# Kernel optimization log

Measured on AMD Instinct MI355X. Metric: run time of the kernel, lower is better.

## Reference

```python
import jax, jax.numpy as jnp
import numpy as np

EPS = 1e-6  # flax nn.LayerNorm default epsilon


def excl_cumsum(a, axis):
    c = jnp.roll(jnp.cumsum(a, axis=axis), 1, axis=axis)
    idx = [slice(None)] * a.ndim
    idx[axis] = slice(0, 1)
    return c.at[tuple(idx)].set(0.0)


def mixed_chunk_attn(q, k, v, n_chunks):
    # Mixed chunk linear attention (https://arxiv.org/pdf/2202.10447.pdf)
    if n_chunks == 1:
        mask = jnp.tri(q.shape[1], q.shape[1], -1, dtype=q.dtype)
        qk = jnp.einsum('bls,bms->blm', q, k) * mask
        return jnp.einsum('blm,bme->ble', qk, v)
    B, L = q.shape[:2]
    C = L // n_chunks
    qc = q.reshape(B, n_chunks, C, -1)
    kc = k.reshape(B, n_chunks, C, -1)
    vc = v.reshape(B, n_chunks, C, -1)
    # global linear attention across chunks (exclusive prefix of kv states)
    kv = excl_cumsum(jnp.einsum('bgcs,bgce->bgse', kc, vc), axis=1)
    glob = jnp.einsum('bgcs,bgse->bgce', qc, kv)
    # local strictly-causal quadratic attention within each chunk
    mask = jnp.tri(C, C, -1, dtype=q.dtype)
    qk = jnp.einsum('bgns,bgms->bgnm', qc, kc) * mask
    loc = jnp.einsum('bgnm,bgme->bgne', qk, vc)
    return (glob + loc).reshape(B, L, -1)


def ln_normalize(x):
    mu = jnp.mean(x, axis=-1, keepdims=True)
    var = jnp.mean(jnp.square(x - mu), axis=-1, keepdims=True)
    return (x - mu) * jax.lax.rsqrt(var + EPS)


def fwblock(x, labels, weights, W1, b1, W2, b2, ln_scale, ln_bias, Wu, bu, step_sizes, n_chunks):
    B, L, D = x.shape
    F = W1.shape[1]

    # slow-weight forward with zero perturbations; grad wrt perturbations gives
    # per-token gradients at each layer's output (rank-one fast-weight updates).
    def slow_loss(p1, p3, p_scale, p_bias):
        h1 = x @ W1 + b1 + p1                    # FWDense(4D) + output perturbation
        h2 = jnp.square(jax.nn.relu(h1))         # FWSquaredRelu (paramless)
        h3 = h2 @ W2 + b2 + p3                   # FWDense(D) + output perturbation
        h4 = ln_normalize(h3) * (ln_scale + p_scale) + (ln_bias + p_bias)
        logits = h4 @ Wu + bu
        ll = -jnp.sum(jax.nn.log_softmax(logits) * labels, axis=-1)
        loss = jnp.sum(weights * ll) / jnp.maximum(jnp.sum(weights), 1e-8)
        return loss, h2

    zeros = (jnp.zeros((B, L, F), x.dtype), jnp.zeros((B, L, D), x.dtype),
             jnp.zeros((B, L, D), x.dtype), jnp.zeros((B, L, D), x.dtype))
    (g1, g3, g_scale, g_bias), h2_slow = jax.grad(
        slow_loss, argnums=(0, 1, 2, 3), has_aux=True)(*zeros)

    # fast-weight forward: rank-one weight updates expressed as causal linear attn
    x1 = x @ W1 + b1 - step_sizes[0] * mixed_chunk_attn(x, x, g1, n_chunks)
    x2 = jnp.square(jax.nn.relu(x1))             # step_sizes[1] unused (no params)
    x3 = x2 @ W2 + b2 - step_sizes[2] * mixed_chunk_attn(x2, h2_slow, g3, n_chunks)
    fast_scale = ln_scale - step_sizes[3] * excl_cumsum(g_scale, axis=1)
    fast_bias = ln_bias - step_sizes[3] * excl_cumsum(g_bias, axis=1)
    x4 = ln_normalize(x3) * fast_scale + fast_bias
    return x4 @ Wu + bu


def setup_inputs():
    key = jax.random.key(0)
    ks = jax.random.split(key, 6)
    B, L, D, V = 2, 2048, 1024, 8192
    F = 4 * D
    x = jax.random.normal(ks[0], (B, L, D), jnp.float32)
    labels = jax.random.uniform(ks[1], (B, L, V), jnp.float32)
    weights = jnp.ones((B, L), jnp.float32)
    W1 = jax.random.normal(ks[2], (D, F), jnp.float32) / np.sqrt(D).astype(np.float32)
    b1 = jnp.zeros((F,), jnp.float32)
    W2 = jax.random.normal(ks[3], (F, D), jnp.float32) / np.sqrt(F).astype(np.float32)
    b2 = jnp.zeros((D,), jnp.float32)
    ln_scale = jnp.ones((D,), jnp.float32)
    ln_bias = jnp.zeros((D,), jnp.float32)
    Wu = jax.random.normal(ks[4], (D, V), jnp.float32) / np.sqrt(D).astype(np.float32)
    bu = jnp.zeros((V,), jnp.float32)
    step_sizes = jnp.full((4,), 0.01, jnp.float32)
    return dict(x=x, labels=labels, weights=weights, W1=W1, b1=b1, W2=W2, b2=b2,
                ln_scale=ln_scale, ln_bias=ln_bias, Wu=Wu, bu=bu,
                step_sizes=step_sizes, n_chunks=16)


def reference(x, labels, weights, W1, b1, W2, b2, ln_scale, ln_bias, Wu, bu, step_sizes, n_chunks):
    return fwblock(x, labels, weights, W1, b1, W2, b2, ln_scale, ln_bias, Wu, bu, step_sizes, n_chunks)
```

## Files before the change

### kernel.cpp

```cpp
#include <hip/hip_runtime.h>
#include <cstdint>

typedef unsigned short ushort_t;
typedef __bf16 bf16x8 __attribute__((ext_vector_type(8)));
typedef float f32x4 __attribute__((ext_vector_type(4)));
typedef ushort_t us8 __attribute__((ext_vector_type(8)));

__device__ __forceinline__ ushort_t f2bf(float f) {
  union { float f; unsigned int u; } v; v.f = f;
  unsigned int u = v.u;
  unsigned int r = (u + 0x7fffu + ((u >> 16) & 1u)) >> 16;
  return (ushort_t)r;
}
__device__ __forceinline__ float bf2f(ushort_t u) {
  union { unsigned int u; float f; } v; v.u = ((unsigned int)u) << 16; return v.f;
}

#define GLOAD16(gp, lp)                                                              \
  __builtin_amdgcn_global_load_lds(                                                  \
      reinterpret_cast<const __attribute__((address_space(1))) unsigned int*>(       \
          reinterpret_cast<uintptr_t>(gp)),                                          \
      reinterpret_cast<__attribute__((address_space(3))) unsigned int*>(             \
          reinterpret_cast<uintptr_t>(lp)),                                          \
      16, 0, 0)

struct GemmP {
  const ushort_t* A; const ushort_t* B;
  int M, N, K;
  long long sA, sB;
  float* outf;   long long sOutF;
  ushort_t* outb; long long sOutB;
  ushort_t* outb2;
  const float* bias;
  const float* auxf; long long sAuxF;
  const ushort_t* auxb;
  const float* steps;
  float* part; int ksplit, Kc, Tt;
};

template <int EPI>
__global__ __launch_bounds__(512, 2) void gemm256(GemmP p) {
  const int nwg = gridDim.x * gridDim.y;
  const int orig = blockIdx.y * gridDim.x + blockIdx.x;
  const int xcd = orig & 7, loc = orig >> 3;
  const int q8 = nwg >> 3, r8 = nwg & 7;
  const int wg = (xcd < r8) ? (xcd * (q8 + 1) + loc) : (r8 * (q8 + 1) + (xcd - r8) * q8 + loc);
  int mt, nt;
  if (EPI == 7) {
    int t_ = wg;
    mt = (int)((sqrtf(8.f * t_ + 1.f) - 1.f) * 0.5f);
    while ((mt + 1) * (mt + 2) / 2 <= t_) mt++;
    while (mt * (mt + 1) / 2 > t_) mt--;
    nt = t_ - mt * (mt + 1) / 2;
  } else {
    nt = wg % gridDim.x; mt = wg / gridDim.x;
  }
  const int m0 = mt * 256, n0 = nt * 256;

  int bz = blockIdx.z, ks = 0;
  if (EPI == 6 || EPI == 7) { bz = blockIdx.z / p.ksplit; ks = blockIdx.z % p.ksplit; }

  const ushort_t* A = p.A + (size_t)bz * p.sA;
  const ushort_t* B = p.B + (size_t)bz * p.sB;

  int kbeg = 0, kend = p.K;
  if (EPI == 6 || EPI == 7) { kbeg = ks * p.Kc; kend = kbeg + p.Kc; }
  else if (EPI == 4) kend = min(p.K, m0 + 256);

  extern __shared__ ushort_t smem[];
  ushort_t* sA = smem;
  ushort_t* sB = smem + 3 * 8192;

  const int tid = threadIdx.x;
  const int wid = tid >> 6, lane = tid & 63;
  const int wm = wid >> 2, wn = wid & 3;

  f32x4 acc[8][4];
#pragma unroll
  for (int i = 0; i < 8; i++)
#pragma unroll
    for (int j = 0; j < 4; j++) acc[i][j] = f32x4{0.f, 0.f, 0.f, 0.f};

  const int lr = lane >> 2;
  const int lcsw = (((lane & 3) ^ ((lr >> 1) & 3)) * 8);
  const int rT0 = wid * 16 + lr;
  const int rT1 = 128 + wid * 16 + lr;
  const ushort_t* gA0 = A + (size_t)(m0 + rT0) * p.K + lcsw;
  const ushort_t* gA1 = A + (size_t)(m0 + rT1) * p.K + lcsw;
  const ushort_t* gB0 = B + (size_t)(n0 + rT0) * p.K + lcsw;
  const ushort_t* gB1 = B + (size_t)(n0 + rT1) * p.K + lcsw;
  ushort_t* lA0 = &sA[wid * 512];
  ushort_t* lA1 = &sA[(8 + wid) * 512];
  ushort_t* lB0 = &sB[wid * 512];
  ushort_t* lB1 = &sB[(8 + wid) * 512];

  const int fr = lane & 15;
  const int q = lane >> 4;
  const int slot = (q ^ ((fr >> 1) & 3)) * 8;
  int offA[8], offB[4];
#pragma unroll
  for (int i = 0; i < 8; i++) offA[i] = (wm * 8 + i) * 512 + fr * 32 + slot;
#pragma unroll
  for (int j = 0; j < 4; j++) offB[j] = (wn * 4 + j) * 512 + fr * 32 + slot;

  const int nIter = (kend - kbeg) >> 5;
  auto stage = [&](int t, int buf) {
    const int kk = kbeg + t * 32;
    const int o = buf * 8192;
    GLOAD16(gA0 + kk, lA0 + o);
    GLOAD16(gA1 + kk, lA1 + o);
    GLOAD16(gB0 + kk, lB0 + o);
    GLOAD16(gB1 + kk, lB1 + o);
  };
  stage(0, 0);
  if (nIter > 1) stage(1, 1);

  for (int t = 0; t < nIter; ++t) {
    if (t + 1 < nIter) { asm volatile("s_waitcnt vmcnt(4)" ::: "memory"); }
    else               { asm volatile("s_waitcnt vmcnt(0)" ::: "memory"); }
    __builtin_amdgcn_s_barrier();
    __builtin_amdgcn_sched_barrier(0);
    if (t + 2 < nIter) stage(t + 2, (t + 2) % 3);
    const int co = (t % 3) * 8192;
    bf16x8 av[8], bv[4];
#pragma unroll
    for (int j = 0; j < 4; j++) bv[j] = *reinterpret_cast<const bf16x8*>(&sB[co + offB[j]]);
#pragma unroll
    for (int i = 0; i < 8; i++) {
      av[i] = *reinterpret_cast<const bf16x8*>(&sA[co + offA[i]]);
#pragma unroll
      for (int j = 0; j < 4; j++)
        acc[i][j] = __builtin_amdgcn_mfma_f32_16x16x32_bf16(av[i], bv[j], acc[i][j], 0, 0, 0);
    }
  }

  const int fq = q;
  float ss = 0.f;
  if (EPI == 4) ss = p.steps[0];
  float* outf = p.outf ? p.outf + (size_t)bz * p.sOutF : nullptr;
  ushort_t* outb = p.outb ? p.outb + (size_t)bz * p.sOutB : nullptr;
  ushort_t* outb2 = p.outb2;
  const ushort_t* auxb = p.auxb ? p.auxb + (size_t)bz * p.sAuxF : nullptr;
  float* partT = nullptr;
  if (EPI == 6) partT = p.part + (size_t)blockIdx.z * p.M * p.N;
  if (EPI == 7) partT = p.part + ((size_t)blockIdx.z * p.Tt + wg) * 65536;

#pragma unroll
  for (int i = 0; i < 8; i++) {
#pragma unroll
    for (int j = 0; j < 4; j++) {
#pragma unroll
      for (int r2 = 0; r2 < 4; r2++) {
        int lrow = wm * 128 + i * 16 + fq * 4 + r2;
        int lcol = wn * 64 + j * 16 + fr;
        int row = m0 + lrow, col = n0 + lcol;
        size_t g = (size_t)row * p.N + col;
        float v = acc[i][j][r2];
        if (EPI == 0) {
          outf[g] = v + (p.bias ? p.bias[col] : 0.f);
        } else if (EPI == 8) {
          outb[g] = f2bf(v + p.bias[col]);
        } else if (EPI == 1) {
          v += p.bias[col];
          outb[g] = f2bf(v);
          float rl = fmaxf(v, 0.f);
          outb2[g] = f2bf(rl * rl);
        } else if (EPI == 2) {
          outb[g] = f2bf(v * 2.f * sqrtf(bf2f(auxb[g])));
        } else if (EPI == 4) {
          float x1 = bf2f(auxb[g]) - ss * v;
          float rl = fmaxf(x1, 0.f);
          outb[g] = f2bf(rl * rl);
        } else if (EPI == 6) {
          partT[g] = v;
        } else if (EPI == 7) {
          partT[lrow * 256 + lcol] = v;
        }
      }
    }
  }
}

template <int EPI>
__global__ __launch_bounds__(256) void gemm_bt(GemmP p) {
  const int nwg = gridDim.x * gridDim.y;
  const int orig = blockIdx.y * gridDim.x + blockIdx.x;
  const int xcd = orig & 7, loc = orig >> 3;
  const int q = nwg >> 3, r = nwg & 7;
  const int wg = (xcd < r) ? (xcd * (q + 1) + loc) : (r * (q + 1) + (xcd - r) * q + loc);
  const int nt = wg % gridDim.x, mt = wg / gridDim.x;
  const int m0 = mt * 128, n0 = nt * 128;
  const int bz = blockIdx.z;

  const ushort_t* A = p.A + (size_t)bz * p.sA;
  const ushort_t* B = p.B + (size_t)bz * p.sB;

  int kend = p.K;
  if (EPI == 5) kend = min(p.K, m0 + 128);

  __shared__ ushort_t sA[3 * 128 * 32];
  __shared__ ushort_t sB[3 * 128 * 32];

  const int tid = threadIdx.x;
  const int wid = tid >> 6, lane = tid & 63;
  const int wm = wid >> 1, wn = wid & 1;

  f32x4 acc[4][4];
#pragma unroll
  for (int i = 0; i < 4; i++)
#pragma unroll
    for (int j = 0; j < 4; j++) acc[i][j] = f32x4{0.f, 0.f, 0.f, 0.f};

  const int lr = lane >> 2;
  const int lc = (lane & 3) * 8;
  const int rA0 = wid * 16 + lr;
  const int rA1 = 64 + wid * 16 + lr;
  const ushort_t* gA0 = A + (size_t)(m0 + rA0) * p.K + lc;
  const ushort_t* gA1 = A + (size_t)(m0 + rA1) * p.K + lc;
  const ushort_t* gB0 = B + (size_t)(n0 + rA0) * p.K + lc;
  const ushort_t* gB1 = B + (size_t)(n0 + rA1) * p.K + lc;
  ushort_t* lA0 = &sA[wid * 512];
  ushort_t* lA1 = &sA[(4 + wid) * 512];
  ushort_t* lB0 = &sB[wid * 512];
  ushort_t* lB1 = &sB[(4 + wid) * 512];

  const int fr = lane & 15;
  const int kb = (lane >> 4) * 8;

  const int nIter = kend >> 5;
  auto stage = [&](int t, int buf) {
    const int kk = t * 32;
    const int o = buf * 4096;
    GLOAD16(gA0 + kk, lA0 + o);
    GLOAD16(gA1 + kk, lA1 + o);
    GLOAD16(gB0 + kk, lB0 + o);
    GLOAD16(gB1 + kk, lB1 + o);
  };
  stage(0, 0);
  if (nIter > 1) stage(1, 1);

  for (int t = 0; t < nIter; ++t) {
    if (t + 1 < nIter) { asm volatile("s_waitcnt vmcnt(4)" ::: "memory"); }
    else               { asm volatile("s_waitcnt vmcnt(0)" ::: "memory"); }
    __builtin_amdgcn_s_barrier();
    __builtin_amdgcn_sched_barrier(0);
    if (t + 2 < nIter) stage(t + 2, (t + 2) % 3);
    const int co = (t % 3) * 4096;
    bf16x8 av[4], bv[4];
#pragma unroll
    for (int i = 0; i < 4; i++) {
      av[i] = *reinterpret_cast<const bf16x8*>(&sA[co + (wm * 64 + i * 16 + fr) * 32 + kb]);
      bv[i] = *reinterpret_cast<const bf16x8*>(&sB[co + (wn * 64 + i * 16 + fr) * 32 + kb]);
    }
#pragma unroll
    for (int i = 0; i < 4; i++)
#pragma unroll
      for (int j = 0; j < 4; j++)
        acc[i][j] = __builtin_amdgcn_mfma_f32_16x16x32_bf16(av[i], bv[j], acc[i][j], 0, 0, 0);
  }

  const int fq = lane >> 4;
  float ss = (EPI == 5) ? p.steps[2] : 0.f;
  float* outf = p.outf ? p.outf + (size_t)bz * p.sOutF : nullptr;
  const float* auxf = p.auxf ? p.auxf + (size_t)bz * p.sAuxF : nullptr;

#pragma unroll
  for (int i = 0; i < 4; i++) {
#pragma unroll
    for (int j = 0; j < 4; j++) {
#pragma unroll
      for (int r2 = 0; r2 < 4; r2++) {
        int row = m0 + wm * 64 + i * 16 + fq * 4 + r2;
        int col = n0 + wn * 64 + j * 16 + fr;
        size_t g = (size_t)row * p.N + col;
        float v = acc[i][j][r2];
        if (EPI == 5) {
          outf[g] = auxf[g] - ss * v;
        } else {
          outf[g] = v + (p.bias ? p.bias[col] : 0.f);
        }
      }
    }
  }
}

__global__ __launch_bounds__(256) void k_comb(const float* part, const float* bias, float* out,
                                              int N, size_t MN, int S) {
  size_t e = ((size_t)blockIdx.x * 256 + threadIdx.x) * 4;
  if (e >= MN) return;
  float4 s = *(const float4*)(part + e);
  for (int p_ = 1; p_ < S; p_++) {
    float4 v = *(const float4*)(part + (size_t)p_ * MN + e);
    s.x += v.x; s.y += v.y; s.z += v.z; s.w += v.w;
  }
  if (bias) {
    int col = (int)(e % (size_t)N);
    s.x += bias[col]; s.y += bias[col + 1]; s.z += bias[col + 2]; s.w += bias[col + 3];
  }
  *(float4*)(out + e) = s;
}

__global__ __launch_bounds__(256) void k_combtri(const float* part, ushort_t* out, int Tt, int S,
                                                 int L) {
  int t = blockIdx.x, bz = blockIdx.y;
  int mt = (int)((sqrtf(8.f * t + 1.f) - 1.f) * 0.5f);
  while ((mt + 1) * (mt + 2) / 2 <= t) mt++;
  while (mt * (mt + 1) / 2 > t) mt--;
  int nt = t - mt * (mt + 1) / 2;
  const float* pb = part + ((size_t)bz * S * Tt + t) * 65536;
  ushort_t* ob = out + (size_t)bz * L * L;
  for (int e4 = threadIdx.x; e4 < 16384; e4 += 256) {
    int e = e4 * 4;
    float4 s = *(const float4*)(pb + e);
    for (int p_ = 1; p_ < S; p_++) {
      float4 v = *(const float4*)(pb + (size_t)p_ * Tt * 65536 + e);
      s.x += v.x; s.y += v.y; s.z += v.z; s.w += v.w;
    }
    int lr = e >> 8, lc2 = e & 255;
    int row = mt * 256 + lr, col = nt * 256 + lc2;
    ushort4 o;
    o.x = (col < row) ? f2bf(s.x) : (ushort_t)0;
    o.y = (col + 1 < row) ? f2bf(s.y) : (ushort_t)0;
    o.z = (col + 2 < row) ? f2bf(s.z) : (ushort_t)0;
    o.w = (col + 3 < row) ? f2bf(s.w) : (ushort_t)0;
    *(ushort4*)(&ob[(size_t)row * L + col]) = o;
  }
}

__global__ __launch_bounds__(256) void k_conv(const float* in, ushort_t* out, size_t n) {
  size_t i = ((size_t)blockIdx.x * 256 + threadIdx.x) * 4;
  if (i >= n) return;
  float4 v = *(const float4*)(in + i);
  out[i] = f2bf(v.x); out[i + 1] = f2bf(v.y); out[i + 2] = f2bf(v.z); out[i + 3] = f2bf(v.w);
}

__global__ __launch_bounds__(256) void k_tconv(const float* in, ushort_t* out, int R, int C) {
  __shared__ float t[32][33];
  int c0 = blockIdx.x * 32, r0 = blockIdx.y * 32;
  int tx = threadIdx.x & 31, ty = threadIdx.x >> 5;
#pragma unroll
  for (int i = ty; i < 32; i += 8) t[i][tx] = in[(size_t)(r0 + i) * C + c0 + tx];
  __syncthreads();
#pragma unroll
  for (int i = ty; i < 32; i += 8) out[(size_t)(c0 + i) * R + r0 + tx] = f2bf(t[tx][i]);
}

__global__ __launch_bounds__(256) void k_wprep(const float* in, ushort_t* outS, ushort_t* outT,
                                               int R, int C) {
  __shared__ float t[32][33];
  int c0 = blockIdx.x * 32, r0 = blockIdx.y * 32;
  int tx = threadIdx.x & 31, ty = threadIdx.x >> 5;
#pragma unroll
  for (int i = ty; i < 32; i += 8) {
    float v = in[(size_t)(r0 + i) * C + c0 + tx];
    t[i][tx] = v;
    outS[(size_t)(r0 + i) * C + c0 + tx] = f2bf(v);
  }
  __syncthreads();
#pragma unroll
  for (int i = ty; i < 32; i += 8) out:
  ;
#pragma unroll
  for (int i = ty; i < 32; i += 8) outT[(size_t)(c0 + i) * R + r0 + tx] = f2bf(t[tx][i]);
}

__global__ __launch_bounds__(256) void k_tb2b(const ushort_t* in, ushort_t* out, int L, int C) {
  __shared__ ushort_t t[32][33];
  int b = blockIdx.z;
  const ushort_t* ib = in + (size_t)b * L * C;
  ushort_t* ob = out + (size_t)b * C * L;
  int c0 = blockIdx.x * 32, l0 = blockIdx.y * 32;
  int tx = threadIdx.x & 31, ty = threadIdx.x >> 5;
#pragma unroll
  for (int i = ty; i < 32; i += 8) t[i][tx] = ib[(size_t)(l0 + i) * C + c0 + tx];
  __syncthreads();
#pragma unroll
  for (int i = ty; i < 32; i += 8) ob[(size_t)(c0 + i) * L + l0 + tx] = t[tx][i];
}

__device__ __forceinline__ void blockRed2(float& a, float& b, float* red) {
#pragma unroll
  for (int o = 32; o; o >>= 1) { a += __shfl_down(a, o); b += __shfl_down(b, o); }
  int w = threadIdx.x >> 6;
  if ((threadIdx.x & 63) == 0) { red[w] = a; red[4 + w] = b; }
  __syncthreads();
  a = red[0] + red[1] + red[2] + red[3];
  b = red[4] + red[5] + red[6] + red[7];
  __syncthreads();
}

__global__ __launch_bounds__(256) void k_lncomb(const float* part, const float* bias,
                                                const float* sc, const float* bi, float* nout,
                                                float* rstd, ushort_t* yb, size_t MN, int D,
                                                int S) {
  __shared__ float red[8];
  int row = blockIdx.x;
  int d = threadIdx.x * 4;
  size_t g = (size_t)row * D + d;
  float4 v = *(const float4*)(part + g);
  for (int s_ = 1; s_ < S; s_++) {
    float4 w = *(const float4*)(part + (size_t)s_ * MN + g);
    v.x += w.x; v.y += w.y; v.z += w.z; v.w += w.w;
  }
  float4 bb = *(const float4*)(bias + d);
  v.x += bb.x; v.y += bb.y; v.z += bb.z; v.w += bb.w;
  float s1 = v.x + v.y + v.z + v.w;
  float s2 = v.x * v.x + v.y * v.y + v.z * v.z + v.w * v.w;
  blockRed2(s1, s2, red);
  float mu = s1 / D;
  float var = s2 / D - mu * mu;
  float rs = rsqrtf(var + 1e-6f);
  float4 nv;
  nv.x = (v.x - mu) * rs; nv.y = (v.y - mu) * rs; nv.z = (v.z - mu) * rs; nv.w = (v.w - mu) * rs;
  *(float4*)(nout + g) = nv;
  float4 scv = *(const float4*)(sc + d);
  float4 biv = *(const float4*)(bi + d);
  ushort4 o;
  o.x = f2bf(nv.x * scv.x + biv.x);
  o.y = f2bf(nv.y * scv.y + biv.y);
  o.z = f2bf(nv.z * scv.z + biv.z);
  o.w = f2bf(nv.w * scv.w + biv.w);
  *(ushort4*)(yb + g) = o;
  if (threadIdx.x == 0) rstd[row] = rs;
}

__global__ __launch_bounds__(256) void k_lnfwd2(const float* X, const float* fs, const float* fb,
                                                ushort_t* yb, int D) {
  __shared__ float red[8];
  int row = blockIdx.x;
  const float* x = X + (size_t)row * D;
  float s = 0.f, s2 = 0.f;
  for (int d = threadIdx.x; d < D; d += 256) { float v = x[d]; s += v; s2 += v * v; }
  blockRed2(s, s2, red);
  float mu = s / D;
  float var = s2 / D - mu * mu;
  float rs = rsqrtf(var + 1e-6f);
  for (int d = threadIdx.x; d < D; d += 256) {
    size_t g = (size_t)row * D + d;
    float nv = (x[d] - mu) * rs;
    yb[g] = f2bf(nv * fs[g] + fb[g]);
  }
}

__global__ __launch_bounds__(256) void k_lnbwd(const float* G, const float* nn, const float* rstd,
                                               const float* sc, ushort_t* g3b, float* gsc, int D) {
  __shared__ float red[8];
  int row = blockIdx.x;
  const float* g = G + (size_t)row * D;
  const float* n_ = nn + (size_t)row * D;
  float sa = 0.f, sb = 0.f;
  for (int d = threadIdx.x; d < D; d += 256) {
    float dn = g[d] * sc[d];
    sa += dn; sb += dn * n_[d];
  }
  blockRed2(sa, sb, red);
  float a = sa / D, b = sb / D, rs = rstd[row];
  for (int d = threadIdx.x; d < D; d += 256) {
    size_t gi = (size_t)row * D + d;
    float dn = g[d] * sc[d];
    g3b[gi] = f2bf(rs * (dn - a - n_[d] * b));
    gsc[gi] = g[d] * n_[d];
  }
}

__global__ __launch_bounds__(256) void k_wsum(const float* w, float* o, int n) {
  __shared__ float red[4];
  float s = 0.f;
  for (int i = threadIdx.x; i < n; i += 256) s += w[i];
#pragma unroll
  for (int d = 32; d; d >>= 1) s += __shfl_down(s, d);
  if ((threadIdx.x & 63) == 0) red[threadIdx.x >> 6] = s;
  __syncthreads();
  if (threadIdx.x == 0) o[0] = fmaxf(red[0] + red[1] + red[2] + red[3], 1e-8f);
}

__global__ __launch_bounds__(256) void k_softgrad(const ushort_t* logits, const float* labels,
                                                  const float* w, const float* wsum,
                                                  ushort_t* dlb, int V) {
  __shared__ float red[8];
  const int row = blockIdx.x;
  const int tid = threadIdx.x;
  const ushort_t* l = logits + (size_t)row * V + tid * 32;
  const float* y = labels + (size_t)row * V + tid * 32;
  float lv[32], yv[32];
#pragma unroll
  for (int i = 0; i < 4; i++) {
    us8 u = *reinterpret_cast<const us8*>(l + i * 8);
#pragma unroll
    for (int j = 0; j < 8; j++) lv[i * 8 + j] = bf2f(u[j]);
  }
#pragma unroll
  for (int i = 0; i < 8; i++) {
    float4 v = *reinterpret_cast<const float4*>(y + i * 4);
    yv[i * 4] = v.x; yv[i * 4 + 1] = v.y; yv[i * 4 + 2] = v.z; yv[i * 4 + 3] = v.w;
  }
  float m = lv[0], t = yv[0];
#pragma unroll
  for (int i = 1; i < 32; i++) { m = fmaxf(m, lv[i]); t += yv[i]; }
#pragma unroll
  for (int o = 32; o; o >>= 1) { m = fmaxf(m, __shfl_down(m, o)); t += __shfl_down(t, o); }
  int wv = tid >> 6;
  if ((tid & 63) == 0) { red[wv] = m; red[4 + wv] = t; }
  __syncthreads();
  m = fmaxf(fmaxf(red[0], red[1]), fmaxf(red[2], red[3]));
  t = red[4] + red[5] + red[6] + red[7];
  __syncthreads();
  float s = 0.f;
#pragma unroll
  for (int i = 0; i < 32; i++) { lv[i] = expf(lv[i] - m); s += lv[i]; }
#pragma unroll
  for (int o = 32; o; o >>= 1) s += __shfl_down(s, o);
  if ((tid & 63) == 0) red[wv] = s;
  __syncthreads();
  s = red[0] + red[1] + red[2] + red[3];
  float c = w[row] / wsum[0];
  float ci = c * t / s;
  ushort_t* dl = dlb + (size_t)row * V + tid * 32;
#pragma unroll
  for (int i = 0; i < 4; i++) {
    us8 o;
#pragma unroll
    for (int j = 0; j < 8; j++) o[j] = f2bf(ci * lv[i * 8 + j] - c * yv[i * 8 + j]);
    *reinterpret_cast<us8*>(dl + i * 8) = o;
  }
}

__global__ __launch_bounds__(256) void k_scanpart(const float* gs, const float* gb, float* ps,
                                                  float* pb, int L, int D) {
  int d = blockIdx.x * 256 + threadIdx.x;
  int seg = blockIdx.y, b = blockIdx.z;
  const int SEGL = L / 16;
  size_t base = ((size_t)b * L + seg * SEGL) * D + d;
  float s1 = 0.f, s2 = 0.f;
  for (int i = 0; i < SEGL; i++) { s1 += gs[base + (size_t)i * D]; s2 += gb[base + (size_t)i * D]; }
  size_t pi = ((size_t)b * 16 + seg) * D + d;
  ps[pi] = s1; pb[pi] = s2;
}

__global__ __launch_bounds__(256) void k_scanapply(const float* gs, const float* gb,
                                                   const float* ps, const float* pb,
                                                   const float* sc, const float* bi,
                                                   const float* steps, float* fs, float* fb,
                                                   int L, int D) {
  int d = blockIdx.x * 256 + threadIdx.x;
  int seg = blockIdx.y, b = blockIdx.z;
  const int SEGL = L / 16;
  float ss = steps[3];
  float rs_ = 0.f, rb_ = 0.f;
  for (int s = 0; s < seg; s++) {
    size_t pi = ((size_t)b * 16 + s) * D + d;
    rs_ += ps[pi]; rb_ += pb[pi];
  }
  float s0 = sc[d], b0 = bi[d];
  size_t base = ((size_t)b * L + seg * SEGL) * D + d;
  for (int i = 0; i < SEGL; i++) {
    size_t g = base + (size_t)i * D;
    fs[g] = s0 - ss * rs_;
    fb[g] = b0 - ss * rb_;
    rs_ += gs[g]; rb_ += gb[g];
  }
}

extern "C" void kernel_launch(void* const* d_in, const int* in_sizes, int n_in, void* d_out,
                              int out_size, void* d_ws, size_t ws_size, hipStream_t stream) {
  const float* x        = (const float*)d_in[0];
  const float* labels   = (const float*)d_in[1];
  const float* weights  = (const float*)d_in[2];
  const float* W1       = (const float*)d_in[3];
  const float* b1       = (const float*)d_in[4];
  const float* W2       = (const float*)d_in[5];
  const float* b2       = (const float*)d_in[6];
  const float* ln_scale = (const float*)d_in[7];
  const float* ln_bias  = (const float*)d_in[8];
  const float* Wu       = (const float*)d_in[9];
  const float* bu       = (const float*)d_in[10];
  const float* steps    = (const float*)d_in[11];

  const int BL = in_sizes[2];
  const int D  = in_sizes[7];
  const int F  = in_sizes[4];
  const int V  = in_sizes[10];
  const int Bb = 2, L = BL / Bb;
  const int T2t = (L / 256) * (L / 256 + 1) / 2;
  const unsigned SMEM = 3 * 8192 * 2 * 2;

  char* ws = (char*)d_ws;
  size_t off = 0;
  auto take = [&](size_t b) { char* p = ws + off; off = (off + b + 255) & ~(size_t)255; return p; };

  ushort_t* xb   = (ushort_t*)take((size_t)BL * D * 2);
  ushort_t* w1t  = (ushort_t*)take((size_t)F * D * 2);
  ushort_t* w2t  = (ushort_t*)take((size_t)D * F * 2);
  ushort_t* w2b  = (ushort_t*)take((size_t)F * D * 2);
  ushort_t* wut  = (ushort_t*)take((size_t)V * D * 2);
  ushort_t* wub  = (ushort_t*)take((size_t)D * V * 2);
  ushort_t* H1b  = (ushort_t*)take((size_t)BL * F * 2);
  ushort_t* H2b  = (ushort_t*)take((size_t)BL * F * 2);
  float*    nbuf = (float*)take((size_t)BL * D * 4);
  float*    rstd = (float*)take((size_t)BL * 4);
  ushort_t* h4b  = (ushort_t*)take((size_t)BL * D * 2);
  float*    wsumb= (float*)take(256);
  float*    G4   = (float*)take((size_t)BL * D * 4);
  float*    gsc  = (float*)take((size_t)BL * D * 4);
  ushort_t* g3b  = (ushort_t*)take((size_t)BL * D * 2);
  ushort_t* g3t  = (ushort_t*)take((size_t)BL * D * 2);
  float*    fs   = (float*)take((size_t)BL * D * 4);
  float*    fb   = (float*)take((size_t)BL * D * 4);
  ushort_t* x4b  = (ushort_t*)take((size_t)BL * D * 2);
  float*    psc  = (float*)take((size_t)Bb * 16 * D * 4);
  float*    pbi  = (float*)take((size_t)Bb * 16 * D * 4);
  char* poolA = take((size_t)BL * V * 4);
  ushort_t* logitsb = (ushort_t*)poolA;
  float*    partA  = (float*)poolA;
  ushort_t* g1b = (ushort_t*)poolA;
  ushort_t* g1t = (ushort_t*)(poolA + (size_t)BL * F * 2);
  ushort_t* S1b = (ushort_t*)(poolA + (size_t)BL * F * 4);
  ushort_t* x2b = (ushort_t*)(poolA + (size_t)BL * F * 4 + (size_t)Bb * L * L * 2);
  char* poolB = take((size_t)BL * V * 2);
  ushort_t* dlb = (ushort_t*)poolB;
  float*    partS1 = (float*)poolB;
  ushort_t* S2b = (ushort_t*)poolB;
  float*    X3  = (float*)(poolB + (size_t)Bb * L * L * 2);
  float*    x3  = (float*)(poolB + (size_t)Bb * L * L * 2 + (size_t)BL * D * 4);

  dim3 blk(256), blk5(512);
  const size_t MN_D = (size_t)BL * D;

  k_conv<<<dim3((unsigned)((size_t)BL * D / 1024)), blk, 0, stream>>>(x, xb, (size_t)BL * D);
  k_tconv<<<dim3(F / 32, D / 32), blk, 0, stream>>>(W1, w1t, D, F);
  k_wprep<<<dim3(D / 32, F / 32), blk, 0, stream>>>(W2, w2b, w2t, F, D);
  k_wprep<<<dim3(V / 32, D / 32), blk, 0, stream>>>(Wu, wub, wut, D, V);

  GemmP p;
  auto clr = [&]() { p = GemmP{}; };

  clr(); p.A = xb; p.B = w1t; p.M = BL; p.N = F; p.K = D;
  p.outb = H1b; p.outb2 = H2b; p.bias = b1;
  gemm256<1><<<dim3(F / 256, BL / 256, 1), blk5, SMEM, stream>>>(p);
  clr(); p.A = H2b; p.B = w2t; p.M = BL; p.N = D; p.K = F;
  p.part = partA; p.ksplit = 4; p.Kc = F / 4;
  gemm256<6><<<dim3(D / 256, BL / 256, 4), blk5, SMEM, stream>>>(p);
  k_lncomb<<<dim3(BL), blk, 0, stream>>>(partA, b2, ln_scale, ln_bias, nbuf, rstd, h4b, MN_D, D, 4);
  clr(); p.A = h4b; p.B = wut; p.M = BL; p.N = V; p.K = D; p.outb = logitsb; p.bias = bu;
  gemm256<8><<<dim3(V / 256, BL / 256, 1), blk5, SMEM, stream>>>(p);
  k_wsum<<<dim3(1), blk, 0, stream>>>(weights, wsumb, BL);
  k_softgrad<<<dim3(BL), blk, 0, stream>>>(logitsb, labels, weights, wsumb, dlb, V);
  clr(); p.A = dlb; p.B = wub; p.M = BL; p.N = D; p.K = V;
  p.part = partA; p.ksplit = 4; p.Kc = V / 4;
  gemm256<6><<<dim3(D / 256, BL / 256, 4), blk5, SMEM, stream>>>(p);
  k_comb<<<dim3((unsigned)(MN_D / 1024)), blk, 0, stream>>>(partA, nullptr, G4, D, MN_D, 4);
  k_lnbwd<<<dim3(BL), blk, 0, stream>>>(G4, nbuf, rstd, ln_scale, g3b, gsc, D);
  clr(); p.A = g3b; p.B = w2b; p.M = BL; p.N = F; p.K = D; p.outb = g1b; p.auxb = H2b;
  gemm256<2><<<dim3(F / 256, BL / 256, 1), blk5, SMEM, stream>>>(p);
  k_tb2b<<<dim3(F / 32, L / 32, Bb), blk, 0, stream>>>(g1b, g1t, L, F);
  k_tb2b<<<dim3(D / 32, L / 32, Bb), blk, 0, stream>>>(g3b, g3t, L, D);
  clr(); p.A = xb; p.B = xb; p.M = L; p.N = L; p.K = D;
  p.sA = (long long)L * D; p.sB = (long long)L * D;
  p.part = partS1; p.ksplit = 2; p.Kc = D / 2; p.Tt = T2t;
  gemm256<7><<<dim3(T2t, 1, Bb * 2), blk5, SMEM, stream>>>(p);
  k_combtri<<<dim3(T2t, Bb), blk, 0, stream>>>(partS1, S1b, T2t, 2, L);
  clr(); p.A = S1b; p.B = g1t; p.M = L; p.N = F; p.K = L;
  p.sA = (long long)L * L; p.sB = (long long)F * L;
  p.outb = x2b; p.sOutB = (long long)L * F; p.auxb = H1b; p.sAuxF = (long long)L * F;
  p.steps = steps;
  gemm256<4><<<dim3(F / 256, L / 256, Bb), blk5, SMEM, stream>>>(p);
  clr(); p.A = x2b; p.B = w2t; p.M = BL; p.N = D; p.K = F;
  p.part = partA; p.ksplit = 4; p.Kc = F / 4;
  gemm256<6><<<dim3(D / 256, BL / 256, 4), blk5, SMEM, stream>>>(p);
  k_comb<<<dim3((unsigned)(MN_D / 1024)), blk, 0, stream>>>(partA, b2, X3, D, MN_D, 4);
  clr(); p.A = x2b; p.B = H2b; p.M = L; p.N = L; p.K = F;
  p.sA = (long long)L * F; p.sB = (long long)L * F;
  p.part = partA; p.ksplit = 4; p.Kc = F / 4; p.Tt = T2t;
  gemm256<7><<<dim3(T2t, 1, Bb * 4), blk5, SMEM, stream>>>(p);
  k_combtri<<<dim3(T2t, Bb), blk, 0, stream>>>(partA, S2b, T2t, 4, L);
  clr(); p.A = S2b; p.B = g3t; p.M = L; p.N = D; p.K = L;
  p.sA = (long long)L * L; p.sB = (long long)D * L;
  p.outf = x3; p.sOutF = (long long)L * D; p.auxf = X3; p.sAuxF = (long long)L * D; p.steps = steps;
  gemm_bt<5><<<dim3(D / 128, L / 128, Bb), blk, 0, stream>>>(p);
  k_scanpart<<<dim3(D / 256, 16, Bb), blk, 0, stream>>>(gsc, G4, psc, pbi, L, D);
  k_scanapply<<<dim3(D / 256, 16, Bb), blk, 0, stream>>>(gsc, G4, psc, pbi, ln_scale, ln_bias,
                                                         steps, fs, fb, L, D);
  k_lnfwd2<<<dim3(BL), blk, 0, stream>>>(x3, fs, fb, x4b, D);
  clr(); p.A = x4b; p.B = wut; p.M = BL; p.N = V; p.K = D; p.outf = (float*)d_out; p.bias = bu;
  gemm256<0><<<dim3(V / 256, BL / 256, 1), blk5, SMEM, stream>>>(p);
}
```

Baseline: 1.083 ms.

## Switch GEMM mainloop to double-buffered BK=64 stages with MFMA priority

Replaces the triple-buffered K=32 pipeline with a double-buffered K=64 pipeline: each iteration prefetches the next 64-wide K tile into the other buffer while computing on the current one, with one barrier per 64 K instead of per 32. LDS fragment loads are grouped before a burst of MFMAs wrapped in s_setprio to favour matrix issue. It also removes a stray dead loop in the weight-prep kernel. The cost is that vmcnt(0) waits now expose the full load latency at the end of each iteration, there is only one tile of lookahead, and LDS use grows from 96KB to 128KB, which may reduce occupancy. K extents must now be multiples of 64.

```diff
diff --git a/kernel.cpp b/kernel.cpp
--- a/kernel.cpp
+++ b/kernel.cpp
@@ -69,7 +69,7 @@
 
   extern __shared__ ushort_t smem[];
   ushort_t* sA = smem;
-  ushort_t* sB = smem + 3 * 8192;
+  ushort_t* sB = smem + 2 * 16384;
 
   const int tid = threadIdx.x;
   const int wid = tid >> 6, lane = tid & 63;
@@ -103,35 +103,49 @@
 #pragma unroll
   for (int j = 0; j < 4; j++) offB[j] = (wn * 4 + j) * 512 + fr * 32 + slot;
 
-  const int nIter = (kend - kbeg) >> 5;
+  const int nIter = (kend - kbeg) >> 6;
   auto stage = [&](int t, int buf) {
-    const int kk = kbeg + t * 32;
-    const int o = buf * 8192;
-    GLOAD16(gA0 + kk, lA0 + o);
-    GLOAD16(gA1 + kk, lA1 + o);
-    GLOAD16(gB0 + kk, lB0 + o);
-    GLOAD16(gB1 + kk, lB1 + o);
+    const int kk = kbeg + t * 64;
+    const int o = buf * 16384;
+#pragma unroll
+    for (int kh = 0; kh < 2; kh++) {
+      const int gk = kk + kh * 32, lo = o + kh * 8192;
+      GLOAD16(gA0 + gk, lA0 + lo);
+      GLOAD16(gA1 + gk, lA1 + lo);
+      GLOAD16(gB0 + gk, lB0 + lo);
+      GLOAD16(gB1 + gk, lB1 + lo);
+    }
   };
   stage(0, 0);
-  if (nIter > 1) stage(1, 1);
-
+  asm volatile("s_waitcnt vmcnt(0)" ::: "memory");
+  __builtin_amdgcn_s_barrier();
+
+  int cur = 0;
   for (int t = 0; t < nIter; ++t) {
-    if (t + 1 < nIter) { asm volatile("s_waitcnt vmcnt(4)" ::: "memory"); }
-    else               { asm volatile("s_waitcnt vmcnt(0)" ::: "memory"); }
-    __builtin_amdgcn_s_barrier();
+    if (t + 1 < nIter) stage(t + 1, cur ^ 1);
     __builtin_amdgcn_sched_barrier(0);
-    if (t + 2 < nIter) stage(t + 2, (t + 2) % 3);
-    const int co = (t % 3) * 8192;
-    bf16x8 av[8], bv[4];
-#pragma unroll
-    for (int j = 0; j < 4; j++) bv[j] = *reinterpret_cast<const bf16x8*>(&sB[co + offB[j]]);
-#pragma unroll
-    for (int i = 0; i < 8; i++) {
-      av[i] = *reinterpret_cast<const bf16x8*>(&sA[co + offA[i]]);
-#pragma unroll
-      for (int j = 0; j < 4; j++)
-        acc[i][j] = __builtin_amdgcn_mfma_f32_16x16x32_bf16(av[i], bv[j], acc[i][j], 0, 0, 0);
+    const int co = cur * 16384;
+#pragma unroll
+    for (int kh = 0; kh < 2; kh++) {
+      const int ko = co + kh * 8192;
+      bf16x8 av[8], bv[4];
+#pragma unroll
+      for (int j = 0; j < 4; j++) bv[j] = *reinterpret_cast<const bf16x8*>(&sB[ko + offB[j]]);
+#pragma unroll
+      for (int i = 0; i < 8; i++) av[i] = *reinterpret_cast<const bf16x8*>(&sA[ko + offA[i]]);
+      __builtin_amdgcn_s_setprio(1);
+#pragma unroll
+      for (int i = 0; i < 8; i++)
+#pragma unroll
+        for (int j = 0; j < 4; j++)
+          acc[i][j] = __builtin_amdgcn_mfma_f32_16x16x32_bf16(av[i], bv[j], acc[i][j], 0, 0, 0);
+      __builtin_amdgcn_s_setprio(0);
     }
+    if (t + 1 < nIter) {
+      asm volatile("s_waitcnt vmcnt(0)" ::: "memory");
+      __builtin_amdgcn_s_barrier();
+    }
+    cur ^= 1;
   }
 
   const int fq = q;
@@ -358,9 +372,6 @@
   }
   __syncthreads();
 #pragma unroll
-  for (int i = ty; i < 32; i += 8) out:
-  ;
-#pragma unroll
   for (int i = ty; i < 32; i += 8) outT[(size_t)(c0 + i) * R + r0 + tx] = f2bf(t[tx][i]);
 }
 
@@ -582,7 +593,7 @@
   const int V  = in_sizes[10];
   const int Bb = 2, L = BL / Bb;
   const int T2t = (L / 256) * (L / 256 + 1) / 2;
-  const unsigned SMEM = 3 * 8192 * 2 * 2;
+  const unsigned SMEM = 2 * 16384 * 2 * 2;
 
   char* ws = (char*)d_ws;
   size_t off = 0;
```

Result: no change. 1.083 ms (-0.0%).

## Restructure GEMM main loop into double-buffered 64-K steps with interleaved half-tile loads

Applied to the files above, without the earlier changes.

The GEMM main loop moves from a triple-buffered 32-wide K pipeline to a double-buffered 64-wide K step. Each step is split into four phases, and each phase issues half of the next tile's global-to-LDS loads (A or B) alongside the MFMA work. Wave priority is raised around the MFMA bursts with s_setprio, and LDS reads are separated from compute by explicit barriers and waitcnts. The aim is finer-grained overlap of memory traffic with matrix math, at the cost of more barriers per K step and the constraint that K ranges be multiples of 64.

```diff
diff --git a/kernel.cpp b/kernel.cpp
--- a/kernel.cpp
+++ b/kernel.cpp
@@ -69,7 +69,7 @@
 
   extern __shared__ ushort_t smem[];
   ushort_t* sA = smem;
-  ushort_t* sB = smem + 3 * 8192;
+  ushort_t* sB = smem + 2 * 16384;
 
   const int tid = threadIdx.x;
   const int wid = tid >> 6, lane = tid & 63;
@@ -103,35 +103,97 @@
 #pragma unroll
   for (int j = 0; j < 4; j++) offB[j] = (wn * 4 + j) * 512 + fr * 32 + slot;
 
-  const int nIter = (kend - kbeg) >> 5;
-  auto stage = [&](int t, int buf) {
-    const int kk = kbeg + t * 32;
-    const int o = buf * 8192;
+  const int nT = (kend - kbeg) >> 6;
+  auto stageA2 = [&](int kk, int o) {
     GLOAD16(gA0 + kk, lA0 + o);
     GLOAD16(gA1 + kk, lA1 + o);
+  };
+  auto stageB2 = [&](int kk, int o) {
     GLOAD16(gB0 + kk, lB0 + o);
     GLOAD16(gB1 + kk, lB1 + o);
   };
-  stage(0, 0);
-  if (nIter > 1) stage(1, 1);
-
-  for (int t = 0; t < nIter; ++t) {
-    if (t + 1 < nIter) { asm volatile("s_waitcnt vmcnt(4)" ::: "memory"); }
-    else               { asm volatile("s_waitcnt vmcnt(0)" ::: "memory"); }
-    __builtin_amdgcn_s_barrier();
+
+  stageA2(kbeg, 0);
+  stageB2(kbeg, 0);
+  stageA2(kbeg + 32, 8192);
+  stageB2(kbeg + 32, 8192);
+  asm volatile("s_waitcnt vmcnt(4)" ::: "memory");
+  __builtin_amdgcn_s_barrier();
+
+  for (int t = 0; t < nT; ++t) {
+    const int co = (t & 1) * 16384;
+    const int no = co ^ 16384;
+    const bool pre = (t + 1 < nT);
+    const int kn = kbeg + (t + 1) * 64;
+    bf16x8 av[4], bv[4];
+
+#pragma unroll
+    for (int j = 0; j < 4; j++) bv[j] = *reinterpret_cast<const bf16x8*>(&sB[co + offB[j]]);
+#pragma unroll
+    for (int i = 0; i < 4; i++) av[i] = *reinterpret_cast<const bf16x8*>(&sA[co + offA[i]]);
+    if (pre) stageA2(kn, no);
+    __builtin_amdgcn_s_barrier();
+    asm volatile("s_waitcnt lgkmcnt(0)" ::: "memory");
     __builtin_amdgcn_sched_barrier(0);
-    if (t + 2 < nIter) stage(t + 2, (t + 2) % 3);
-    const int co = (t % 3) * 8192;
-    bf16x8 av[8], bv[4];
-#pragma unroll
-    for (int j = 0; j < 4; j++) bv[j] = *reinterpret_cast<const bf16x8*>(&sB[co + offB[j]]);
-#pragma unroll
-    for (int i = 0; i < 8; i++) {
-      av[i] = *reinterpret_cast<const bf16x8*>(&sA[co + offA[i]]);
+    __builtin_amdgcn_s_setprio(1);
+#pragma unroll
+    for (int i = 0; i < 4; i++)
 #pragma unroll
       for (int j = 0; j < 4; j++)
         acc[i][j] = __builtin_amdgcn_mfma_f32_16x16x32_bf16(av[i], bv[j], acc[i][j], 0, 0, 0);
-    }
+    __builtin_amdgcn_s_setprio(0);
+    __builtin_amdgcn_s_barrier();
+
+#pragma unroll
+    for (int i = 0; i < 4; i++) av[i] = *reinterpret_cast<const bf16x8*>(&sA[co + offA[4 + i]]);
+    if (pre) stageB2(kn, no);
+    __builtin_amdgcn_s_barrier();
+    asm volatile("s_waitcnt lgkmcnt(0)" ::: "memory");
+    __builtin_amdgcn_sched_barrier(0);
+    __builtin_amdgcn_s_setprio(1);
+#pragma unroll
+    for (int i = 0; i < 4; i++)
+#pragma unroll
+      for (int j = 0; j < 4; j++)
+        acc[4 + i][j] = __builtin_amdgcn_mfma_f32_16x16x32_bf16(av[i], bv[j], acc[4 + i][j], 0, 0, 0);
+    __builtin_amdgcn_s_setprio(0);
+    if (pre) { asm volatile("s_waitcnt vmcnt(4)" ::: "memory"); }
+    else     { asm volatile("s_waitcnt vmcnt(0)" ::: "memory"); }
+    __builtin_amdgcn_s_barrier();
+
+    const int c1 = co + 8192;
+#pragma unroll
+    for (int j = 0; j < 4; j++) bv[j] = *reinterpret_cast<const bf16x8*>(&sB[c1 + offB[j]]);
+#pragma unroll
+    for (int i = 0; i < 4; i++) av[i] = *reinterpret_cast<const bf16x8*>(&sA[c1 + offA[i]]);
+    if (pre) stageA2(kn + 32, no + 8192);
+    __builtin_amdgcn_s_barrier();
+    asm volatile("s_waitcnt lgkmcnt(0)" ::: "memory");
+    __builtin_amdgcn_sched_barrier(0);
+    __builtin_amdgcn_s_setprio(1);
+#pragma unroll
+    for (int i = 0; i < 4; i++)
+#pragma unroll
+      for (int j = 0; j < 4; j++)
+        acc[i][j] = __builtin_amdgcn_mfma_f32_16x16x32_bf16(av[i], bv[j], acc[i][j], 0, 0, 0);
+    __builtin_amdgcn_s_setprio(0);
+    __builtin_amdgcn_s_barrier();
+
+#pragma unroll
+    for (int i = 0; i < 4; i++) av[i] = *reinterpret_cast<const bf16x8*>(&sA[c1 + offA[4 + i]]);
+    if (pre) stageB2(kn + 32, no + 8192);
+    __builtin_amdgcn_s_barrier();
+    asm volatile("s_waitcnt lgkmcnt(0)" ::: "memory");
+    __builtin_amdgcn_sched_barrier(0);
+    __builtin_amdgcn_s_setprio(1);
+#pragma unroll
+    for (int i = 0; i < 4; i++)
+#pragma unroll
+      for (int j = 0; j < 4; j++)
+        acc[4 + i][j] = __builtin_amdgcn_mfma_f32_16x16x32_bf16(av[i], bv[j], acc[4 + i][j], 0, 0, 0);
+    __builtin_amdgcn_s_setprio(0);
+    if (pre) { asm volatile("s_waitcnt vmcnt(4)" ::: "memory"); }
+    __builtin_amdgcn_s_barrier();
   }
 
   const int fq = q;
@@ -358,9 +420,6 @@
   }
   __syncthreads();
 #pragma unroll
-  for (int i = ty; i < 32; i += 8) out:
-  ;
-#pragma unroll
   for (int i = ty; i < 32; i += 8) outT[(size_t)(c0 + i) * R + r0 + tx] = f2bf(t[tx][i]);
 }
 
@@ -582,7 +641,7 @@
   const int V  = in_sizes[10];
   const int Bb = 2, L = BL / Bb;
   const int T2t = (L / 256) * (L / 256 + 1) / 2;
-  const unsigned SMEM = 3 * 8192 * 2 * 2;
+  const unsigned SMEM = 2 * 16384 * 2 * 2;
 
   char* ws = (char*)d_ws;
   size_t off = 0;
```

Result: no change. 1.075 ms (-0.8%).

## Deepen GEMM LDS pipeline to four stages with MFMA priority boost

Applied to the files above, without the earlier changes.

Both GEMM kernels move from a 3-buffer to a 4-buffer LDS ring, prefetching three K-tiles ahead. The wait and barrier move to the end of each iteration, and s_setprio is raised around the MFMA block so more global-load latency is hidden. LDS use grows to 128KB per block for gemm256, which may limit occupancy. The S2 triangular split-K also drops from 4 to 2 splits, halving partial traffic and combine work but giving fewer blocks.

```diff
diff --git a/kernel.cpp b/kernel.cpp
--- a/kernel.cpp
+++ b/kernel.cpp
@@ -69,7 +69,7 @@
 
   extern __shared__ ushort_t smem[];
   ushort_t* sA = smem;
-  ushort_t* sB = smem + 3 * 8192;
+  ushort_t* sB = smem + 4 * 8192;
 
   const int tid = threadIdx.x;
   const int wid = tid >> 6, lane = tid & 63;
@@ -103,35 +103,43 @@
 #pragma unroll
   for (int j = 0; j < 4; j++) offB[j] = (wn * 4 + j) * 512 + fr * 32 + slot;
 
-  const int nIter = (kend - kbeg) >> 5;
-  auto stage = [&](int t, int buf) {
+  const int nT = (kend - kbeg) >> 5;
+  auto stage4 = [&](int t) {
     const int kk = kbeg + t * 32;
-    const int o = buf * 8192;
+    const int o = (t & 3) * 8192;
     GLOAD16(gA0 + kk, lA0 + o);
     GLOAD16(gA1 + kk, lA1 + o);
     GLOAD16(gB0 + kk, lB0 + o);
     GLOAD16(gB1 + kk, lB1 + o);
   };
-  stage(0, 0);
-  if (nIter > 1) stage(1, 1);
-
-  for (int t = 0; t < nIter; ++t) {
-    if (t + 1 < nIter) { asm volatile("s_waitcnt vmcnt(4)" ::: "memory"); }
-    else               { asm volatile("s_waitcnt vmcnt(0)" ::: "memory"); }
-    __builtin_amdgcn_s_barrier();
+  stage4(0);
+  if (nT > 1) stage4(1);
+  if (nT > 2) stage4(2);
+  if (nT > 2)      { asm volatile("s_waitcnt vmcnt(8)" ::: "memory"); }
+  else if (nT > 1) { asm volatile("s_waitcnt vmcnt(4)" ::: "memory"); }
+  else             { asm volatile("s_waitcnt vmcnt(0)" ::: "memory"); }
+  __builtin_amdgcn_s_barrier();
+
+  for (int t = 0; t < nT; ++t) {
+    const int co = (t & 3) * 8192;
+    if (t + 3 < nT) stage4(t + 3);
     __builtin_amdgcn_sched_barrier(0);
-    if (t + 2 < nIter) stage(t + 2, (t + 2) % 3);
-    const int co = (t % 3) * 8192;
     bf16x8 av[8], bv[4];
 #pragma unroll
     for (int j = 0; j < 4; j++) bv[j] = *reinterpret_cast<const bf16x8*>(&sB[co + offB[j]]);
 #pragma unroll
-    for (int i = 0; i < 8; i++) {
-      av[i] = *reinterpret_cast<const bf16x8*>(&sA[co + offA[i]]);
+    for (int i = 0; i < 8; i++) av[i] = *reinterpret_cast<const bf16x8*>(&sA[co + offA[i]]);
+    __builtin_amdgcn_s_setprio(1);
+#pragma unroll
+    for (int i = 0; i < 8; i++)
 #pragma unroll
       for (int j = 0; j < 4; j++)
         acc[i][j] = __builtin_amdgcn_mfma_f32_16x16x32_bf16(av[i], bv[j], acc[i][j], 0, 0, 0);
-    }
+    __builtin_amdgcn_s_setprio(0);
+    if (t + 3 < nT)      { asm volatile("s_waitcnt vmcnt(8)" ::: "memory"); }
+    else if (t + 2 < nT) { asm volatile("s_waitcnt vmcnt(4)" ::: "memory"); }
+    else if (t + 1 < nT) { asm volatile("s_waitcnt vmcnt(0)" ::: "memory"); }
+    __builtin_amdgcn_s_barrier();
   }
 
   const int fq = q;
@@ -198,8 +206,8 @@
   int kend = p.K;
   if (EPI == 5) kend = min(p.K, m0 + 128);
 
-  __shared__ ushort_t sA[3 * 128 * 32];
-  __shared__ ushort_t sB[3 * 128 * 32];
+  __shared__ ushort_t sA[4 * 128 * 32];
+  __shared__ ushort_t sB[4 * 128 * 32];
 
   const int tid = threadIdx.x;
   const int wid = tid >> 6, lane = tid & 63;
@@ -228,35 +236,43 @@
   const int kb = (lane >> 4) * 8;
 
   const int nIter = kend >> 5;
-  auto stage = [&](int t, int buf) {
+  auto stage = [&](int t) {
     const int kk = t * 32;
-    const int o = buf * 4096;
+    const int o = (t & 3) * 4096;
     GLOAD16(gA0 + kk, lA0 + o);
     GLOAD16(gA1 + kk, lA1 + o);
     GLOAD16(gB0 + kk, lB0 + o);
     GLOAD16(gB1 + kk, lB1 + o);
   };
-  stage(0, 0);
-  if (nIter > 1) stage(1, 1);
+  stage(0);
+  if (nIter > 1) stage(1);
+  if (nIter > 2) stage(2);
+  if (nIter > 2)      { asm volatile("s_waitcnt vmcnt(8)" ::: "memory"); }
+  else if (nIter > 1) { asm volatile("s_waitcnt vmcnt(4)" ::: "memory"); }
+  else                { asm volatile("s_waitcnt vmcnt(0)" ::: "memory"); }
+  __builtin_amdgcn_s_barrier();
 
   for (int t = 0; t < nIter; ++t) {
-    if (t + 1 < nIter) { asm volatile("s_waitcnt vmcnt(4)" ::: "memory"); }
-    else               { asm volatile("s_waitcnt vmcnt(0)" ::: "memory"); }
-    __builtin_amdgcn_s_barrier();
+    const int co = (t & 3) * 4096;
+    if (t + 3 < nIter) stage(t + 3);
     __builtin_amdgcn_sched_barrier(0);
-    if (t + 2 < nIter) stage(t + 2, (t + 2) % 3);
-    const int co = (t % 3) * 4096;
     bf16x8 av[4], bv[4];
 #pragma unroll
     for (int i = 0; i < 4; i++) {
       av[i] = *reinterpret_cast<const bf16x8*>(&sA[co + (wm * 64 + i * 16 + fr) * 32 + kb]);
       bv[i] = *reinterpret_cast<const bf16x8*>(&sB[co + (wn * 64 + i * 16 + fr) * 32 + kb]);
     }
+    __builtin_amdgcn_s_setprio(1);
 #pragma unroll
     for (int i = 0; i < 4; i++)
 #pragma unroll
       for (int j = 0; j < 4; j++)
         acc[i][j] = __builtin_amdgcn_mfma_f32_16x16x32_bf16(av[i], bv[j], acc[i][j], 0, 0, 0);
+    __builtin_amdgcn_s_setprio(0);
+    if (t + 3 < nIter)      { asm volatile("s_waitcnt vmcnt(8)" ::: "memory"); }
+    else if (t + 2 < nIter) { asm volatile("s_waitcnt vmcnt(4)" ::: "memory"); }
+    else if (t + 1 < nIter) { asm volatile("s_waitcnt vmcnt(0)" ::: "memory"); }
+    __builtin_amdgcn_s_barrier();
   }
 
   const int fq = lane >> 4;
@@ -358,9 +374,6 @@
   }
   __syncthreads();
 #pragma unroll
-  for (int i = ty; i < 32; i += 8) out:
-  ;
-#pragma unroll
   for (int i = ty; i < 32; i += 8) outT[(size_t)(c0 + i) * R + r0 + tx] = f2bf(t[tx][i]);
 }
 
@@ -582,7 +595,7 @@
   const int V  = in_sizes[10];
   const int Bb = 2, L = BL / Bb;
   const int T2t = (L / 256) * (L / 256 + 1) / 2;
-  const unsigned SMEM = 3 * 8192 * 2 * 2;
+  const unsigned SMEM = 4 * 8192 * 2 * 2;
 
   char* ws = (char*)d_ws;
   size_t off = 0;
@@ -670,9 +683,9 @@
   k_comb<<<dim3((unsigned)(MN_D / 1024)), blk, 0, stream>>>(partA, b2, X3, D, MN_D, 4);
   clr(); p.A = x2b; p.B = H2b; p.M = L; p.N = L; p.K = F;
   p.sA = (long long)L * F; p.sB = (long long)L * F;
-  p.part = partA; p.ksplit = 4; p.Kc = F / 4; p.Tt = T2t;
-  gemm256<7><<<dim3(T2t, 1, Bb * 4), blk5, SMEM, stream>>>(p);
-  k_combtri<<<dim3(T2t, Bb), blk, 0, stream>>>(partA, S2b, T2t, 4, L);
+  p.part = partA; p.ksplit = 2; p.Kc = F / 2; p.Tt = T2t;
+  gemm256<7><<<dim3(T2t, 1, Bb * 2), blk5, SMEM, stream>>>(p);
+  k_combtri<<<dim3(T2t, Bb), blk, 0, stream>>>(partA, S2b, T2t, 2, L);
   clr(); p.A = S2b; p.B = g3t; p.M = L; p.N = D; p.K = L;
   p.sA = (long long)L * L; p.sB = (long long)D * L;
   p.outf = x3; p.sOutF = (long long)L * D; p.auxf = X3; p.sAuxF = (long long)L * D; p.steps = steps;
```

Result: faster. 1.036 ms (-4.3%).
